# Kernel optimization log

Measured on AMD Instinct MI355X. Metric: run time of the kernel, lower is better.

The kernel has to match this reference:

```python
import jax, jax.numpy as jnp
import numpy as np
import math

B, S, D, H = 2, 2048, 1024, 16
DK = D // H


def setup_inputs() -> dict:
    key = jax.random.key(0)
    ks = jax.random.split(key, 12)
    std = 1.0 / math.sqrt(D)
    inp = {
        "query": jax.random.normal(ks[0], (B, S, D), jnp.float32),
        "key": jax.random.normal(ks[1], (B, S, D), jnp.float32),
        "value": jax.random.normal(ks[2], (B, S, D), jnp.float32),
        # causal mask, broadcast over batch and heads
        "mask": jnp.tril(jnp.ones((S, S), jnp.int32))[None, None, :, :],
        # nn.Linear weights are [out_features, in_features]
        "Wq": jax.random.uniform(ks[3], (D, D), jnp.float32, -std, std),
        "bq": jax.random.uniform(ks[4], (D,), jnp.float32, -std, std),
        "Wk": jax.random.uniform(ks[5], (D, D), jnp.float32, -std, std),
        "bk": jax.random.uniform(ks[6], (D,), jnp.float32, -std, std),
        "Wv": jax.random.uniform(ks[7], (D, D), jnp.float32, -std, std),
        "bv": jax.random.uniform(ks[8], (D,), jnp.float32, -std, std),
        "Wo": jax.random.uniform(ks[9], (D, D), jnp.float32, -std, std),
        "bo": jax.random.uniform(ks[10], (D,), jnp.float32, -std, std),
    }
    return inp


def reference(query, key, value, mask, Wq, bq, Wk, bk, Wv, bv, Wo, bo):
    q = query @ Wq.T + bq  # [B,S,D]
    k = key @ Wk.T + bk
    v = value @ Wv.T + bv
    # Faithful to the original: a raw view (reshape), NOT a head-transpose split.
    q = q.reshape(B, H, S, DK)
    k = k.reshape(B, H, S, DK)
    v = v.reshape(B, H, S, DK)
    scores = jnp.einsum("bhqd,bhkd->bhqk", q, k) / math.sqrt(DK)
    scores = jnp.where(mask == 0, jnp.float32(-1e9), scores)
    weights = jax.nn.softmax(scores, axis=-1)
    # dropout(p=0.1) is identity in eval mode
    context = jnp.einsum("bhqk,bhkd->bhqd", weights, v)
    context = context.transpose(0, 2, 1, 3).reshape(B, S, D)
    return context @ Wo.T + bo
```

## Files before the change

kernel.cpp:

```cpp
#include <hip/hip_runtime.h>
#include <hip/hip_bf16.h>

#define BB 2
#define SS 2048
#define DD 1024
#define HH 16
#define DKK 64

typedef __attribute__((ext_vector_type(4))) float  f32x4;
typedef __attribute__((ext_vector_type(8))) short  s16x8;
typedef __attribute__((ext_vector_type(4))) short  s16x4;
typedef __attribute__((ext_vector_type(4))) float  fvec4;
typedef __attribute__((ext_vector_type(2))) unsigned int u32x2;

__device__ __forceinline__ short f2bs(float f) {
    union { __hip_bfloat16 b; short s; } u;
    u.b = __float2bfloat16(f);
    return u.s;
}

__device__ __forceinline__ unsigned cvtpk(float lo, float hi) {
    unsigned r;
    asm("v_cvt_pk_bf16_f32 %0, %1, %2" : "=v"(r) : "v"(lo), "v"(hi));
    return r;
}

__device__ __forceinline__ void gload_lds16(const short* g, short* l) {
    __builtin_amdgcn_global_load_lds((const __attribute__((address_space(1))) void*)g,
                                     (__attribute__((address_space(3))) void*)l, 16, 0, 0);
}

__global__ __launch_bounds__(256) void cvt_all(
    const float* __restrict__ q,  const float* __restrict__ k,  const float* __restrict__ v,
    const float* __restrict__ wq, const float* __restrict__ wk, const float* __restrict__ wv,
    const float* __restrict__ wo,
    short* __restrict__ qo,  short* __restrict__ ko,  short* __restrict__ vo,
    short* __restrict__ wqo, short* __restrict__ wko, short* __restrict__ wvo,
    short* __restrict__ woo)
{
    const float* src; short* dst; int n;
    switch (blockIdx.y) {
        case 0: src = q;  dst = qo;  n = BB * SS * DD; break;
        case 1: src = k;  dst = ko;  n = BB * SS * DD; break;
        case 2: src = v;  dst = vo;  n = BB * SS * DD; break;
        case 3: src = wq; dst = wqo; n = DD * DD; break;
        case 4: src = wk; dst = wko; n = DD * DD; break;
        case 5: src = wv; dst = wvo; n = DD * DD; break;
        default: src = wo; dst = woo; n = DD * DD; break;
    }
    int i = (blockIdx.x * 256 + threadIdx.x) * 8;
    const int stride = gridDim.x * 256 * 8;
    for (; i < n; i += stride) {
        fvec4 a = *(const fvec4*)&src[i];
        fvec4 b = *(const fvec4*)&src[i + 4];
        s16x8 o;
        o[0] = f2bs(a[0]); o[1] = f2bs(a[1]); o[2] = f2bs(a[2]); o[3] = f2bs(a[3]);
        o[4] = f2bs(b[0]); o[5] = f2bs(b[1]); o[6] = f2bs(b[2]); o[7] = f2bs(b[3]);
        *(s16x8*)&dst[i] = o;
    }
}

template<int BN, int NXSH, bool OUTF32>
__global__ __launch_bounds__(256) void gemm_nt_v2(
    const short* __restrict__ A0, const short* __restrict__ A1, const short* __restrict__ A2,
    const short* __restrict__ B0, const short* __restrict__ B1, const short* __restrict__ B2,
    const float* __restrict__ c0, const float* __restrict__ c1, const float* __restrict__ c2,
    void* __restrict__ O0, void* __restrict__ O1, void* __restrict__ O2,
    float os0, float os1, float os2,
    int ppx, int NY, int KL, int N, int K)
{
    const int d   = blockIdx.x;
    const int xcd = d & 7;
    const int s   = d >> 3;
    const int x   = s & ((1 << NXSH) - 1);
    const int pl  = s >> NXSH;
    const int panel = xcd * ppx + pl;
    const int y   = panel % NY;
    const int z   = panel / NY;

    const short* A    = z == 0 ? A0 : (z == 1 ? A1 : A2);
    const short* Bw   = z == 0 ? B0 : (z == 1 ? B1 : B2);
    const float* bias = z == 0 ? c0 : (z == 1 ? c1 : c2);
    void* Cp          = z == 0 ? O0 : (z == 1 ? O1 : O2);
    const float oscale = z == 0 ? os0 : (z == 1 ? os1 : os2);

    __shared__ short As[128][64];
    __shared__ short Bs[BN][64];

    const int tid  = threadIdx.x;
    const int lane = tid & 63;
    const int wid  = tid >> 6;
    const int r16  = lane & 15;
    const int g    = lane >> 4;
    const int m0   = y * 128;
    const int n0   = x * BN;
    constexpr int MR = 4;
    constexpr int NR = BN / 32;
    const int wr   = (wid >> 1) * 64;
    const int wc   = (wid & 1) * (BN / 2);
    const int srow8 = lane >> 3;
    const int c8    = lane & 7;

    f32x4 acc[MR][NR];
#pragma unroll
    for (int mi = 0; mi < MR; ++mi)
#pragma unroll
        for (int ni = 0; ni < NR; ++ni) acc[mi][ni] = (f32x4){0.f, 0.f, 0.f, 0.f};

    const int csrc = (c8 ^ srow8) * 8;
    const int nk = KL >> 6;
#pragma unroll 1
    for (int kt = 0; kt < nk; ++kt) {
        const int k0 = kt * 64;
        if (kt) __syncthreads();
#pragma unroll
        for (int q = 0; q < 4; ++q) {
            const int r = wid * 32 + q * 8 + srow8;
            gload_lds16(&A[(size_t)(m0 + r) * K + k0 + csrc], &As[wid * 32 + q * 8][0]);
        }
#pragma unroll
        for (int q = 0; q < BN / 32; ++q) {
            const int r = wid * (BN / 4) + q * 8 + srow8;
            gload_lds16(&Bw[(size_t)(n0 + r) * K + k0 + csrc], &Bs[wid * (BN / 4) + q * 8][0]);
        }
        __syncthreads();

#pragma unroll
        for (int kk = 0; kk < 2; ++kk) {
            s16x8 af[MR], bf[NR];
#pragma unroll
            for (int mi = 0; mi < MR; ++mi) {
                const int row = wr + mi * 16 + r16;
                af[mi] = *(const s16x8*)&As[row][((kk * 4 + g) ^ (row & 7)) * 8];
            }
#pragma unroll
            for (int ni = 0; ni < NR; ++ni) {
                const int row = wc + ni * 16 + r16;
                bf[ni] = *(const s16x8*)&Bs[row][((kk * 4 + g) ^ (row & 7)) * 8];
            }
#pragma unroll
            for (int mi = 0; mi < MR; ++mi)
#pragma unroll
                for (int ni = 0; ni < NR; ++ni)
                    acc[mi][ni] = __builtin_amdgcn_mfma_f32_16x16x32_bf16(
                        af[mi], bf[ni], acc[mi][ni], 0, 0, 0);
        }
    }

#pragma unroll
    for (int ni = 0; ni < NR; ++ni) {
        const int col = n0 + wc + ni * 16 + r16;
        const float bv = bias ? bias[col] : 0.f;
#pragma unroll
        for (int mi = 0; mi < MR; ++mi) {
#pragma unroll
            for (int r = 0; r < 4; ++r) {
                const int row = m0 + wr + mi * 16 + g * 4 + r;
                const float vv = (acc[mi][ni][r] + bv) * oscale;
                if constexpr (OUTF32)
                    ((float*)Cp)[(size_t)row * N + col] = vv;
                else
                    ((short*)Cp)[(size_t)row * N + col] = f2bs(vv);
            }
        }
    }
}

__global__ __launch_bounds__(256) void mha_transpose_v(
    const short* __restrict__ vp, short* __restrict__ vT)
{
    const int st = blockIdx.x;
    const int bh = blockIdx.y;
    const short* src = vp + (size_t)bh * SS * DKK;
    short*       dst = vT + (size_t)bh * SS * DKK;
    const int tid = threadIdx.x;
#pragma unroll
    for (int i = 0; i < 2; ++i) {
        const int c  = tid + i * 256;
        const int dk = c >> 3;
        const int sc = c & 7;
        const int s0 = st * 64 + sc * 8;
        s16x8 v;
#pragma unroll
        for (int j = 0; j < 8; ++j) v[j] = src[(size_t)(s0 + j) * DKK + dk];
        *(s16x8*)&dst[(size_t)dk * SS + s0] = v;
    }
}

__global__ __launch_bounds__(256, 2) void mha_attn(
    const short* __restrict__ qp, const short* __restrict__ kp,
    const short* __restrict__ vT, short* __restrict__ ctx)
{
    __shared__ short Ks[64][64];
    __shared__ short Vs[64][64];
    __shared__ short P[4][16][72];

    const int tid  = threadIdx.x;
    const int wid  = tid >> 6;
    const int lane = tid & 63;
    const int r16  = lane & 15;
    const int g    = lane >> 4;

    const int bh  = blockIdx.x;
    const int bxp = blockIdx.y;
    const int b   = bh >> 4;
    const int h   = bh & 15;

    const short* Qh = qp + (size_t)bh * SS * DKK;
    const short* Kh = kp + (size_t)bh * SS * DKK;
    const short* Vh = vT + (size_t)bh * SS * DKK;

    const int srow = lane >> 3;
    const int csw  = (((lane & 7) ^ srow) & 7) * 8;
    const int r0   = wid * 16;

#pragma unroll 1
    for (int t = 0; t < 2; ++t) {
        const int grp = t ? (31 - bxp) : bxp;
        const int qr0 = grp * 64 + wid * 16;
        const int nkt = grp + 1;

        const s16x8 qf0 = *(const s16x8*)&Qh[(size_t)(qr0 + r16) * DKK + g * 8];
        const s16x8 qf1 = *(const s16x8*)&Qh[(size_t)(qr0 + r16) * DKK + 32 + g * 8];

        f32x4 po[4];
#pragma unroll
        for (int i = 0; i < 4; ++i) po[i] = (f32x4){0.f, 0.f, 0.f, 0.f};
        float lsum = 0.f;

#pragma unroll 1
        for (int j = 0; j < nkt; ++j) {
            const int k0 = j * 64;
            __syncthreads();
            {
                const int rowA = r0 + srow;
                const int rowB = rowA + 8;
                gload_lds16(&Kh[(size_t)(k0 + rowA) * DKK + csw], &Ks[r0][0]);
                gload_lds16(&Kh[(size_t)(k0 + rowB) * DKK + csw], &Ks[r0 + 8][0]);
                gload_lds16(&Vh[(size_t)rowA * SS + k0 + csw], &Vs[r0][0]);
                gload_lds16(&Vh[(size_t)rowB * SS + k0 + csw], &Vs[r0 + 8][0]);
            }
            __syncthreads();

            f32x4 sc[4];
            __builtin_amdgcn_s_setprio(1);
#pragma unroll
            for (int cg = 0; cg < 4; ++cg) {
                const int R  = cg * 16 + r16;
                const int sw = R & 7;
                const s16x8 kf0 = *(const s16x8*)&Ks[R][((g ^ sw) & 7) * 8];
                const s16x8 kf1 = *(const s16x8*)&Ks[R][(((4 + g) ^ sw) & 7) * 8];
                f32x4 tt = (f32x4){0.f, 0.f, 0.f, 0.f};
                tt = __builtin_amdgcn_mfma_f32_16x16x32_bf16(kf0, qf0, tt, 0, 0, 0);
                tt = __builtin_amdgcn_mfma_f32_16x16x32_bf16(kf1, qf1, tt, 0, 0, 0);
                sc[cg] = tt;
            }
            __builtin_amdgcn_s_setprio(0);

            if (j == nkt - 1) {
#pragma unroll
                for (int cg = 0; cg < 4; ++cg)
#pragma unroll
                    for (int r = 0; r < 4; ++r)
                        if (k0 + cg * 16 + g * 4 + r > qr0 + r16) sc[cg][r] = -1e9f;
            }
#pragma unroll
            for (int cg = 0; cg < 4; ++cg) {
                const float p0 = __expf(sc[cg][0]);
                const float p1 = __expf(sc[cg][1]);
                const float p2 = __expf(sc[cg][2]);
                const float p3 = __expf(sc[cg][3]);
                lsum += (p0 + p1) + (p2 + p3);
                u32x2 w;
                w[0] = cvtpk(p0, p1);
                w[1] = cvtpk(p2, p3);
                *(u32x2*)&P[wid][r16][cg * 16 + g * 4] = w;
            }
            const s16x8 pf0 = *(const s16x8*)&P[wid][r16][g * 8];
            const s16x8 pf1 = *(const s16x8*)&P[wid][r16][32 + g * 8];

            __builtin_amdgcn_s_setprio(1);
#pragma unroll
            for (int dg = 0; dg < 4; ++dg) {
                const int Rv = dg * 16 + r16;
                const int sw = Rv & 7;
                const s16x8 vf0 = *(const s16x8*)&Vs[Rv][((g ^ sw) & 7) * 8];
                const s16x8 vf1 = *(const s16x8*)&Vs[Rv][(((4 + g) ^ sw) & 7) * 8];
                po[dg] = __builtin_amdgcn_mfma_f32_16x16x32_bf16(pf0, vf0, po[dg], 0, 0, 0);
                po[dg] = __builtin_amdgcn_mfma_f32_16x16x32_bf16(pf1, vf1, po[dg], 0, 0, 0);
            }
            __builtin_amdgcn_s_setprio(0);
        }

        lsum += __shfl_xor(lsum, 16);
        lsum += __shfl_xor(lsum, 32);
        const float linv = __builtin_amdgcn_rcpf(lsum);
        float rowinv[4];
#pragma unroll
        for (int r = 0; r < 4; ++r)
            rowinv[r] = __shfl(linv, g * 4 + r);
#pragma unroll
        for (int dg = 0; dg < 4; ++dg)
#pragma unroll
            for (int r = 0; r < 4; ++r) {
                const int srw = qr0 + g * 4 + r;
                const float v = po[dg][r] * rowinv[r];
                ctx[((size_t)(b * SS + srw)) * DD + h * 64 + dg * 16 + r16] = f2bs(v);
            }
    }
}

extern "C" void kernel_launch(void* const* d_in, const int* in_sizes, int n_in,
                              void* d_out, int out_size, void* d_ws, size_t ws_size,
                              hipStream_t stream) {
    const float* query = (const float*)d_in[0];
    const float* key   = (const float*)d_in[1];
    const float* value = (const float*)d_in[2];
    const float* Wq = (const float*)d_in[4];
    const float* bq = (const float*)d_in[5];
    const float* Wk = (const float*)d_in[6];
    const float* bk = (const float*)d_in[7];
    const float* Wv = (const float*)d_in[8];
    const float* bv = (const float*)d_in[9];
    const float* Wo = (const float*)d_in[10];
    const float* bo = (const float*)d_in[11];
    float* out = (float*)d_out;

    const size_t elems = (size_t)BB * SS * DD;
    const size_t wel   = (size_t)DD * DD;
    short* qx  = (short*)d_ws;
    short* kx  = qx + elems;
    short* vx  = kx + elems;
    short* wqx = vx + elems;
    short* wkx = wqx + wel;
    short* wvx = wkx + wel;
    short* wox = wvx + wel;
    short* qp  = wox + wel;
    short* kp  = qp + elems;
    short* vp  = kp + elems;
    short* vT  = qx;
    short* ctx = vx;

    cvt_all<<<dim3(1024, 7), 256, 0, stream>>>(query, key, value, Wq, Wk, Wv, Wo,
                                               qx, kx, vx, wqx, wkx, wvx, wox);
    gemm_nt_v2<128, 3, false><<<dim3(768), 256, 0, stream>>>(
        qx, kx, vx, wqx, wkx, wvx, bq, bk, bv, qp, kp, vp,
        0.125f, 1.0f, 1.0f, 12, 32, 1024, DD, DD);
    mha_transpose_v<<<dim3(SS / 64, BB * HH), 256, 0, stream>>>(vp, vT);
    mha_attn<<<dim3(BB * HH, 16), 256, 0, stream>>>(qp, kp, vT, ctx);
    gemm_nt_v2<64, 4, true><<<dim3(512), 256, 0, stream>>>(
        ctx, ctx, ctx, wox, wox, wox, bo, bo, bo, out, out, out,
        1.0f, 1.0f, 1.0f, 4, 32, 1024, DD, DD);
}
```

Baseline: 120.3 us.

## Rewrite attention with 32x32 MFMA, 2-wave blocks, and XCD-aware tile mapping

The attention kernel switches from 16x16x32 MFMA tiles in 4-wave blocks to 32x32x16 MFMA tiles in 2-wave blocks. Each wave now owns 32 query rows, and each block handles a single query tile instead of a paired causal tile set. The 1D grid of 1024 blocks is remapped so blocks of the same head land on the same XCD, and short and long causal tiles are interleaved for balance. The larger MFMA tiles are meant to cut LDS fragment reads per FLOP and improve L2 locality for K/V. In exchange, per-wave register pressure rises and the block count and workload balance change.

```diff
diff --git a/kernel.cpp b/kernel.cpp
--- a/kernel.cpp
+++ b/kernel.cpp
@@ -8,6 +8,7 @@
 #define DKK 64
 
 typedef __attribute__((ext_vector_type(4))) float  f32x4;
+typedef __attribute__((ext_vector_type(16))) float f32x16;
 typedef __attribute__((ext_vector_type(8))) short  s16x8;
 typedef __attribute__((ext_vector_type(4))) short  s16x4;
 typedef __attribute__((ext_vector_type(4))) float  fvec4;
@@ -187,22 +188,26 @@
     }
 }
 
-__global__ __launch_bounds__(256, 2) void mha_attn(
+__global__ __launch_bounds__(128) void mha_attn(
     const short* __restrict__ qp, const short* __restrict__ kp,
     const short* __restrict__ vT, short* __restrict__ ctx)
 {
     __shared__ short Ks[64][64];
     __shared__ short Vs[64][64];
-    __shared__ short P[4][16][72];
+    __shared__ short P[2][32][64];
 
     const int tid  = threadIdx.x;
     const int wid  = tid >> 6;
     const int lane = tid & 63;
-    const int r16  = lane & 15;
-    const int g    = lane >> 4;
-
-    const int bh  = blockIdx.x;
-    const int bxp = blockIdx.y;
+    const int q31  = lane & 31;
+    const int hi   = lane >> 5;
+
+    const int lin = blockIdx.x;
+    const int xcd = lin & 7;
+    const int idx = lin >> 3;
+    const int bh  = (xcd << 2) | (idx >> 5);
+    const int u   = idx & 31;
+    const int qt  = (u & 1) ? (31 - (u >> 1)) : (u >> 1);
     const int b   = bh >> 4;
     const int h   = bh & 15;
 
@@ -212,102 +217,107 @@
 
     const int srow = lane >> 3;
     const int csw  = (((lane & 7) ^ srow) & 7) * 8;
-    const int r0   = wid * 16;
+
+    const int qrow = qt * 64 + wid * 32 + q31;
+    const int nkt  = qt + 1;
+
+    s16x8 qf[4];
+#pragma unroll
+    for (int ks = 0; ks < 4; ++ks)
+        qf[ks] = *(const s16x8*)&Qh[(size_t)qrow * DKK + ks * 16 + hi * 8];
+
+    f32x16 po[2];
+#pragma unroll
+    for (int vb = 0; vb < 2; ++vb)
+#pragma unroll
+        for (int r = 0; r < 16; ++r) po[vb][r] = 0.f;
+    float lsum = 0.f;
 
 #pragma unroll 1
-    for (int t = 0; t < 2; ++t) {
-        const int grp = t ? (31 - bxp) : bxp;
-        const int qr0 = grp * 64 + wid * 16;
-        const int nkt = grp + 1;
-
-        const s16x8 qf0 = *(const s16x8*)&Qh[(size_t)(qr0 + r16) * DKK + g * 8];
-        const s16x8 qf1 = *(const s16x8*)&Qh[(size_t)(qr0 + r16) * DKK + 32 + g * 8];
-
-        f32x4 po[4];
-#pragma unroll
-        for (int i = 0; i < 4; ++i) po[i] = (f32x4){0.f, 0.f, 0.f, 0.f};
-        float lsum = 0.f;
-
-#pragma unroll 1
-        for (int j = 0; j < nkt; ++j) {
-            const int k0 = j * 64;
-            __syncthreads();
-            {
-                const int rowA = r0 + srow;
-                const int rowB = rowA + 8;
-                gload_lds16(&Kh[(size_t)(k0 + rowA) * DKK + csw], &Ks[r0][0]);
-                gload_lds16(&Kh[(size_t)(k0 + rowB) * DKK + csw], &Ks[r0 + 8][0]);
-                gload_lds16(&Vh[(size_t)rowA * SS + k0 + csw], &Vs[r0][0]);
-                gload_lds16(&Vh[(size_t)rowB * SS + k0 + csw], &Vs[r0 + 8][0]);
-            }
-            __syncthreads();
-
-            f32x4 sc[4];
-            __builtin_amdgcn_s_setprio(1);
-#pragma unroll
-            for (int cg = 0; cg < 4; ++cg) {
-                const int R  = cg * 16 + r16;
-                const int sw = R & 7;
-                const s16x8 kf0 = *(const s16x8*)&Ks[R][((g ^ sw) & 7) * 8];
-                const s16x8 kf1 = *(const s16x8*)&Ks[R][(((4 + g) ^ sw) & 7) * 8];
-                f32x4 tt = (f32x4){0.f, 0.f, 0.f, 0.f};
-                tt = __builtin_amdgcn_mfma_f32_16x16x32_bf16(kf0, qf0, tt, 0, 0, 0);
-                tt = __builtin_amdgcn_mfma_f32_16x16x32_bf16(kf1, qf1, tt, 0, 0, 0);
-                sc[cg] = tt;
-            }
-            __builtin_amdgcn_s_setprio(0);
-
-            if (j == nkt - 1) {
-#pragma unroll
-                for (int cg = 0; cg < 4; ++cg)
-#pragma unroll
-                    for (int r = 0; r < 4; ++r)
-                        if (k0 + cg * 16 + g * 4 + r > qr0 + r16) sc[cg][r] = -1e9f;
-            }
-#pragma unroll
-            for (int cg = 0; cg < 4; ++cg) {
-                const float p0 = __expf(sc[cg][0]);
-                const float p1 = __expf(sc[cg][1]);
-                const float p2 = __expf(sc[cg][2]);
-                const float p3 = __expf(sc[cg][3]);
-                lsum += (p0 + p1) + (p2 + p3);
+    for (int j = 0; j < nkt; ++j) {
+        const int k0 = j * 64;
+        __syncthreads();
+#pragma unroll
+        for (int qq = 0; qq < 4; ++qq) {
+            const int rA = wid * 32 + qq * 8 + srow;
+            gload_lds16(&Kh[(size_t)(k0 + rA) * DKK + csw], &Ks[wid * 32 + qq * 8][0]);
+            gload_lds16(&Vh[(size_t)rA * SS + k0 + csw],    &Vs[wid * 32 + qq * 8][0]);
+        }
+        __syncthreads();
+
+        f32x16 sc[2];
+        __builtin_amdgcn_s_setprio(1);
+#pragma unroll
+        for (int kb = 0; kb < 2; ++kb) {
+            const int R = kb * 32 + q31;
+            f32x16 t;
+#pragma unroll
+            for (int r = 0; r < 16; ++r) t[r] = 0.f;
+#pragma unroll
+            for (int ks = 0; ks < 4; ++ks) {
+                const s16x8 kf = *(const s16x8*)&Ks[R][((ks * 2 + hi) ^ (R & 7)) * 8];
+                t = __builtin_amdgcn_mfma_f32_32x32x16_bf16(kf, qf[ks], t, 0, 0, 0);
+            }
+            sc[kb] = t;
+        }
+        __builtin_amdgcn_s_setprio(0);
+
+        if (j == nkt - 1) {
+#pragma unroll
+            for (int kb = 0; kb < 2; ++kb)
+#pragma unroll
+                for (int r = 0; r < 16; ++r) {
+                    const int key = k0 + kb * 32 + (r & 3) + 8 * (r >> 2) + 4 * hi;
+                    if (key > qrow) sc[kb][r] = -1e9f;
+                }
+        }
+#pragma unroll
+        for (int kb = 0; kb < 2; ++kb) {
+            float p[16];
+#pragma unroll
+            for (int r = 0; r < 16; ++r) {
+                p[r] = __expf(sc[kb][r]);
+                lsum += p[r];
+            }
+#pragma unroll
+            for (int qd = 0; qd < 4; ++qd) {
                 u32x2 w;
-                w[0] = cvtpk(p0, p1);
-                w[1] = cvtpk(p2, p3);
-                *(u32x2*)&P[wid][r16][cg * 16 + g * 4] = w;
-            }
-            const s16x8 pf0 = *(const s16x8*)&P[wid][r16][g * 8];
-            const s16x8 pf1 = *(const s16x8*)&P[wid][r16][32 + g * 8];
-
-            __builtin_amdgcn_s_setprio(1);
-#pragma unroll
-            for (int dg = 0; dg < 4; ++dg) {
-                const int Rv = dg * 16 + r16;
-                const int sw = Rv & 7;
-                const s16x8 vf0 = *(const s16x8*)&Vs[Rv][((g ^ sw) & 7) * 8];
-                const s16x8 vf1 = *(const s16x8*)&Vs[Rv][(((4 + g) ^ sw) & 7) * 8];
-                po[dg] = __builtin_amdgcn_mfma_f32_16x16x32_bf16(pf0, vf0, po[dg], 0, 0, 0);
-                po[dg] = __builtin_amdgcn_mfma_f32_16x16x32_bf16(pf1, vf1, po[dg], 0, 0, 0);
-            }
-            __builtin_amdgcn_s_setprio(0);
-        }
-
-        lsum += __shfl_xor(lsum, 16);
-        lsum += __shfl_xor(lsum, 32);
-        const float linv = __builtin_amdgcn_rcpf(lsum);
-        float rowinv[4];
-#pragma unroll
-        for (int r = 0; r < 4; ++r)
-            rowinv[r] = __shfl(linv, g * 4 + r);
-#pragma unroll
-        for (int dg = 0; dg < 4; ++dg)
-#pragma unroll
-            for (int r = 0; r < 4; ++r) {
-                const int srw = qr0 + g * 4 + r;
-                const float v = po[dg][r] * rowinv[r];
-                ctx[((size_t)(b * SS + srw)) * DD + h * 64 + dg * 16 + r16] = f2bs(v);
-            }
-    }
+                w[0] = cvtpk(p[qd * 4 + 0], p[qd * 4 + 1]);
+                w[1] = cvtpk(p[qd * 4 + 2], p[qd * 4 + 3]);
+                const int kc = kb * 4 + qd;
+                *(u32x2*)&P[wid][q31][((kc ^ (q31 & 7)) * 8) + hi * 4] = w;
+            }
+        }
+        s16x8 pf[4];
+#pragma unroll
+        for (int ks2 = 0; ks2 < 4; ++ks2)
+            pf[ks2] = *(const s16x8*)&P[wid][q31][((ks2 * 2 + hi) ^ (q31 & 7)) * 8];
+
+        __builtin_amdgcn_s_setprio(1);
+#pragma unroll
+        for (int vb = 0; vb < 2; ++vb) {
+            const int Rv = vb * 32 + q31;
+#pragma unroll
+            for (int ks2 = 0; ks2 < 4; ++ks2) {
+                const s16x8 vf = *(const s16x8*)&Vs[Rv][((ks2 * 2 + hi) ^ (Rv & 7)) * 8];
+                po[vb] = __builtin_amdgcn_mfma_f32_32x32x16_bf16(vf, pf[ks2], po[vb], 0, 0, 0);
+            }
+        }
+        __builtin_amdgcn_s_setprio(0);
+    }
+
+    lsum += __shfl_xor(lsum, 32);
+    const float linv = __builtin_amdgcn_rcpf(lsum);
+    short* crow = &ctx[((size_t)(b * SS + qrow)) * DD + h * 64];
+#pragma unroll
+    for (int vb = 0; vb < 2; ++vb)
+#pragma unroll
+        for (int qd = 0; qd < 4; ++qd) {
+            u32x2 w;
+            w[0] = cvtpk(po[vb][qd * 4 + 0] * linv, po[vb][qd * 4 + 1] * linv);
+            w[1] = cvtpk(po[vb][qd * 4 + 2] * linv, po[vb][qd * 4 + 3] * linv);
+            *(u32x2*)&crow[vb * 32 + qd * 8 + hi * 4] = w;
+        }
 }
 
 extern "C" void kernel_launch(void* const* d_in, const int* in_sizes, int n_in,
@@ -347,7 +357,7 @@
         qx, kx, vx, wqx, wkx, wvx, bq, bk, bv, qp, kp, vp,
         0.125f, 1.0f, 1.0f, 12, 32, 1024, DD, DD);
     mha_transpose_v<<<dim3(SS / 64, BB * HH), 256, 0, stream>>>(vp, vT);
-    mha_attn<<<dim3(BB * HH, 16), 256, 0, stream>>>(qp, kp, vT, ctx);
+    mha_attn<<<dim3(1024), 128, 0, stream>>>(qp, kp, vT, ctx);
     gemm_nt_v2<64, 4, true><<<dim3(512), 256, 0, stream>>>(
         ctx, ctx, ctx, wox, wox, wox, bo, bo, bo, out, out, out,
         1.0f, 1.0f, 1.0f, 4, 32, 1024, DD, DD);
```

Result: slower. 139.2 us (+15.6%).
